# Kernel tuning notes

Measured on AMD Instinct MI355X. Metric: run time of the kernel, lower is better.

Reference implementation:

```python
import jax, jax.numpy as jnp
import numpy as np

N, E, D, V, MAX_EDGES, G, ITERS = 50000, 200000, 128, 2000, 3, 256, 2


def _mlp3(h, W1, b1, W2, b2, W3, b3):
    h = jax.nn.relu(h @ W1 + b1)
    h = jax.nn.relu(h @ W2 + b2)
    return jax.nn.relu(h @ W3 + b3)


def _enc(ids, emb, W1, b1, W2, b2):
    h = emb[ids]
    h = jax.nn.relu(h @ W1 + b1)
    return jax.nn.relu(h @ W2 + b2)


def setup_inputs():
    key = jax.random.key(0)
    ks = iter(jax.random.split(key, 64))

    def p(shape):
        return jax.random.normal(next(ks), shape, jnp.float32) * 0.02

    inp = {
        'x': jax.random.randint(next(ks), (N,), 0, V),
        'edge_index': jax.random.randint(next(ks), (2, E), 0, N),
        'edge_attr': jax.random.randint(next(ks), (E,), 0, MAX_EDGES),
        'batch_vec': jnp.sort(jax.random.randint(next(ks), (N,), 0, G)),
        'emb_node': p((V, 2 * D)), 'Wn1': p((2 * D, D)), 'bn1': jnp.zeros((D,), jnp.float32),
        'Wn2': p((D, D)), 'bn2': jnp.zeros((D,), jnp.float32),
        'emb_edge': p((MAX_EDGES, 2 * D)), 'We1': p((2 * D, D)), 'be1': jnp.zeros((D,), jnp.float32),
        'We2': p((D, D)), 'be2': jnp.zeros((D,), jnp.float32),
    }
    for tag in ('p', 'c', 'f'):  # parent_agg, child_agg, final_agg 3-layer MLPs
        inp['W' + tag + '1'] = p((3 * D, 2 * D)); inp['b' + tag + '1'] = jnp.zeros((2 * D,), jnp.float32)
        inp['W' + tag + '2'] = p((2 * D, D)); inp['b' + tag + '2'] = jnp.zeros((D,), jnp.float32)
        inp['W' + tag + '3'] = p((D, D)); inp['b' + tag + '3'] = jnp.zeros((D,), jnp.float32)
    inp['Wo1'] = p((D, 4 * D)); inp['bo1'] = jnp.zeros((4 * D,), jnp.float32)
    inp['Wo2'] = p((4 * D, 8 * D)); inp['bo2'] = jnp.zeros((8 * D,), jnp.float32)
    return inp


def reference(x, edge_index, edge_attr, batch_vec, emb_node, Wn1, bn1, Wn2, bn2,
              emb_edge, We1, be1, We2, be2,
              Wp1, bp1, Wp2, bp2, Wp3, bp3,
              Wc1, bc1, Wc2, bc2, Wc3, bc3,
              Wf1, bf1, Wf2, bf2, Wf3, bf3,
              Wo1, bo1, Wo2, bo2):
    nodes = _enc(x, emb_node, Wn1, bn1, Wn2, bn2)       # [N, D]
    ea = _enc(edge_attr, emb_edge, We1, be1, We2, be2)  # [E, D]
    src, dst = edge_index[0], edge_index[1]
    # both aggregations normalize by degree of edge_index[0] (as in the source)
    deg = jax.ops.segment_sum(jnp.ones((E,), nodes.dtype), src, num_segments=N)
    deg_inv = jnp.where(deg > 0, 1.0 / deg, 0.0)[:, None]  # [N, 1]
    for _ in range(ITERS):
        # parent agg: flow source_to_target -> x_i = nodes[dst], x_j = nodes[src], sum at dst
        mp = _mlp3(jnp.concatenate([nodes[dst], nodes[src], ea], axis=1), Wp1, bp1, Wp2, bp2, Wp3, bp3)
        fi = deg_inv * jax.ops.segment_sum(mp, dst, num_segments=N)
        # child agg: flow target_to_source -> x_i = nodes[src], x_j = nodes[dst], sum at src
        mc = _mlp3(jnp.concatenate([nodes[src], nodes[dst], ea], axis=1), Wc1, bc1, Wc2, bc2, Wc3, bc3)
        fo = deg_inv * jax.ops.segment_sum(mc, src, num_segments=N)
        upd = _mlp3(jnp.concatenate([nodes, fi, fo], axis=1), Wf1, bf1, Wf2, bf2, Wf3, bf3)
        nodes = nodes + upd
    h = jax.nn.relu(nodes @ Wo1 + bo1)
    h = jax.nn.relu(h @ Wo2 + bo2)                      # [N, 8D]
    return jax.ops.segment_max(h, batch_vec, num_segments=G)  # global max pool [G, 8D]
```

## Files before the change

### kernel.cpp

```cpp
#include <hip/hip_runtime.h>

#define NN 50000
#define NE 200000
#define DD 128
#define GG 256
#define NITERS 2
#define NBINS 50176
#define NPART 196

typedef unsigned short u16;
typedef unsigned int u32;
typedef __bf16 bf16x8 __attribute__((ext_vector_type(8)));
typedef float f32x4 __attribute__((ext_vector_type(4)));

union U16x8 { uint4 u; bf16x8 v; u16 s[8]; };

__device__ __forceinline__ u16 f2b(float f) {
    u32 u = __float_as_uint(f);
    return (u16)((u + 0x7FFFu + ((u >> 16) & 1u)) >> 16);
}
__device__ __forceinline__ float b2f(u16 s) { return __uint_as_float(((u32)s) << 16); }

__device__ __forceinline__ uint2 pack4(const float* v) {
    uint2 r;
    r.x = (u32)f2b(v[0]) | ((u32)f2b(v[1]) << 16);
    r.y = (u32)f2b(v[2]) | ((u32)f2b(v[3]) << 16);
    return r;
}

__device__ __forceinline__ void gload_lds16(const void* g, void* lds) {
    __builtin_amdgcn_global_load_lds((const __attribute__((address_space(1))) void*)g,
                                     (__attribute__((address_space(3))) void*)lds, 16, 0, 0);
}

__device__ __forceinline__ int xcd_swz(int orig, int nwg) {
    int q = nwg >> 3, r = nwg & 7;
    int x = orig & 7, loc = orig >> 3;
    return (x < r ? x * (q + 1) : r * (q + 1) + (x - r) * q) + loc;
}

template<int K, int NL, int EPI, bool RELU, int LDN>
__global__ __launch_bounds__(256) void expand_k(
    const u16* __restrict__ A, const uint4* __restrict__ wfrag,
    const float* __restrict__ bias, float* __restrict__ of, u16* __restrict__ ob,
    float* __restrict__ zf, int M)
{
    constexpr int KS = K / 32;
    __shared__ uint4 smem[K * 16];
    const int t = threadIdx.x, l = t & 63, wv = t >> 6;
    const int mh = wv >> 1, nh = wv & 1;
    const int mblk = blockIdx.x;
    const int c = blockIdx.y;

    #pragma unroll
    for (int i = 0; i < K / 16; ++i) {
        int s = t + 256 * i;
        int ln = s & 63, mt = (s >> 6) & 7, ksl = s >> 9;
        int row = mblk * 128 + mt * 16 + (ln & 15);
        if (row >= M) row = M - 1;
        int kk = ksl * 32 + (ln >> 4) * 8;
        gload_lds16(A + (size_t)row * K + kk, &smem[s - ln]);
    }
    if (zf) {
        #pragma unroll
        for (int i = 0; i < 4; ++i) {
            int f = t + 256 * i;
            int row = f >> 3, c4 = f & 7;
            int grow = mblk * 128 + row;
            if (grow < M) {
                float4 z; z.x = 0.f; z.y = 0.f; z.z = 0.f; z.w = 0.f;
                *(float4*)(zf + (size_t)grow * 128 + c * 32 + c4 * 4) = z;
            }
        }
    }
    __syncthreads();

    f32x4 acc[4][4] = {};
    #pragma unroll
    for (int ksl = 0; ksl < KS; ++ksl) {
        uint4 wa[4];
        #pragma unroll
        for (int mi = 0; mi < 4; ++mi)
            wa[mi] = wfrag[(size_t)((c * KS + ksl) * 8 + mh * 4 + mi) * 64 + l];
        bf16x8 bn[4];
        #pragma unroll
        for (int ni = 0; ni < 4; ++ni) { U16x8 u; u.u = smem[(ksl * 8 + nh * 4 + ni) * 64 + l]; bn[ni] = u.v; }
        #pragma unroll
        for (int mi = 0; mi < 4; ++mi) {
            U16x8 u; u.u = wa[mi];
            #pragma unroll
            for (int ni = 0; ni < 4; ++ni)
                acc[mi][ni] = __builtin_amdgcn_mfma_f32_16x16x32_bf16(u.v, bn[ni], acc[mi][ni], 0, 0, 0);
        }
    }
    float4 bb[4];
    #pragma unroll
    for (int mi = 0; mi < 4; ++mi) {
        if (bias) bb[mi] = *(const float4*)(bias + c * 128 + mh * 64 + mi * 16 + 4 * (l >> 4));
        else { bb[mi].x = 0.f; bb[mi].y = 0.f; bb[mi].z = 0.f; bb[mi].w = 0.f; }
    }
    #pragma unroll
    for (int ni = 0; ni < 4; ++ni) {
        int node = mblk * 128 + nh * 64 + ni * 16 + (l & 15);
        if (node >= M) continue;
        #pragma unroll
        for (int mi = 0; mi < 4; ++mi) {
            int col = c * 128 + mh * 64 + mi * 16 + 4 * (l >> 4);
            float v[4];
            const float* bf = &bb[mi].x;
            #pragma unroll
            for (int r = 0; r < 4; ++r) {
                v[r] = acc[mi][ni][r] + bf[r];
                if (RELU) v[r] = fmaxf(v[r], 0.f);
            }
            if (EPI == 0) {
                *(uint2*)(ob + (size_t)node * LDN + col) = pack4(v);
            } else {
                size_t a = (size_t)node * 128 + col;
                if (EPI == 2) {
                    float4 old = *(const float4*)(of + a);
                    v[0] += old.x; v[1] += old.y; v[2] += old.z; v[3] += old.w;
                }
                float4 s4; s4.x = v[0]; s4.y = v[1]; s4.z = v[2]; s4.w = v[3];
                *(float4*)(of + a) = s4;
                *(uint2*)(ob + a) = pack4(v);
            }
        }
    }
}

struct SrcBf16 {
    static constexpr bool DIRECT = true;
    const u16* A; int K;
    __device__ const void* gaddr(int row, int kk) const { return A + (size_t)row * K + kk; }
    __device__ bf16x8 operator()(int row, int kk) const {
        U16x8 u; u.u = *(const uint4*)(A + (size_t)row * K + kk); return u.v;
    }
};
struct SrcEnc {
    static constexpr bool DIRECT = false;
    const float* emb; const int* xids;
    __device__ const void* gaddr(int, int) const { return nullptr; }
    __device__ bf16x8 operator()(int row, int kk) const {
        int n = xids[row];
        const float* p = emb + (size_t)n * 256 + kk;
        float4 f0 = *(const float4*)p, f1 = *(const float4*)(p + 4);
        U16x8 r;
        r.s[0]=f2b(f0.x); r.s[1]=f2b(f0.y); r.s[2]=f2b(f0.z); r.s[3]=f2b(f0.w);
        r.s[4]=f2b(f1.x); r.s[5]=f2b(f1.y); r.s[6]=f2b(f1.z); r.s[7]=f2b(f1.w);
        return r.v;
    }
};
struct SrcUpd {
    static constexpr bool DIRECT = false;
    const float* nodes; const float* fi; const float* fo; const int* deg;
    __device__ const void* gaddr(int, int) const { return nullptr; }
    __device__ bf16x8 operator()(int row, int kk) const {
        const float* s; float sc = 1.f;
        if (kk < 128) s = nodes + (size_t)row * 128 + kk;
        else {
            int d = deg[row];
            sc = d > 0 ? 1.f / (float)d : 0.f;
            s = (kk < 256) ? fi + (size_t)row * 128 + (kk - 128)
                           : fo + (size_t)row * 128 + (kk - 256);
        }
        float4 f0 = *(const float4*)s, f1 = *(const float4*)(s + 4);
        U16x8 r;
        r.s[0]=f2b(f0.x*sc); r.s[1]=f2b(f0.y*sc); r.s[2]=f2b(f0.z*sc); r.s[3]=f2b(f0.w*sc);
        r.s[4]=f2b(f1.x*sc); r.s[5]=f2b(f1.y*sc); r.s[6]=f2b(f1.z*sc); r.s[7]=f2b(f1.w*sc);
        return r.v;
    }
};

struct EpiArgs { float* of; u16* ob; const int* idx; int ldN; };

template<int KDIM, int NBLK, int EPI, bool RELU, class SRC>
__global__ __launch_bounds__(256) void gemm_k(SRC src, const uint4* __restrict__ wfrag,
                                              const float* __restrict__ bias,
                                              EpiArgs ea, int M)
{
    constexpr int KS = KDIM / 32;
    constexpr int NPANEL = KDIM / 64;
    __shared__ uint4 smem[2048];
    const int t = threadIdx.x;
    const int l = t & 63;
    const int wv = t >> 6;
    const int mh = wv >> 1, nh = wv & 1;
    const int ell = xcd_swz(blockIdx.x, gridDim.x);
    const int mblk = ell / NBLK, nblk = ell % NBLK;

    f32x4 acc[4][4] = {};

    for (int p = 0; p < NPANEL; ++p) {
        __syncthreads();
        if constexpr (SRC::DIRECT) {
            #pragma unroll
            for (int i = 0; i < 4; ++i) {
                int s = t + 256 * i;
                int ln = s & 63, mt = (s >> 6) & 7, ksl = s >> 9;
                int row = mblk * 128 + mt * 16 + (ln & 15);
                if (row >= M) row = M - 1;
                int kk = p * 64 + ksl * 32 + (ln >> 4) * 8;
                gload_lds16(src.gaddr(row, kk), &smem[s - ln]);
            }
        } else {
            #pragma unroll
            for (int i = 0; i < 4; ++i) {
                int s = t + 256 * i;
                int ln = s & 63, mt = (s >> 6) & 7, ksl = s >> 9;
                int row = mblk * 128 + mt * 16 + (ln & 15);
                if (row >= M) row = M - 1;
                int kk = p * 64 + ksl * 32 + (ln >> 4) * 8;
                U16x8 u; u.v = src(row, kk);
                smem[s] = u.u;
            }
        }
        {
            const uint4* wp = wfrag + (size_t)(nblk * KS + 2 * p) * 512;
            #pragma unroll
            for (int i = 0; i < 4; ++i) {
                int s = t + 256 * i;
                gload_lds16(wp + s, &smem[1024 + (s - (s & 63))]);
            }
        }
        __syncthreads();
        #pragma unroll
        for (int ksl = 0; ksl < 2; ++ksl) {
            bf16x8 a[4], b[4];
            #pragma unroll
            for (int mi = 0; mi < 4; ++mi) { U16x8 u; u.u = smem[(ksl*8 + mh*4 + mi)*64 + l]; a[mi] = u.v; }
            #pragma unroll
            for (int ni = 0; ni < 4; ++ni) { U16x8 u; u.u = smem[1024 + (ksl*8 + nh*4 + ni)*64 + l]; b[ni] = u.v; }
            #pragma unroll
            for (int mi = 0; mi < 4; ++mi)
                #pragma unroll
                for (int ni = 0; ni < 4; ++ni)
                    acc[mi][ni] = __builtin_amdgcn_mfma_f32_16x16x32_bf16(a[mi], b[ni], acc[mi][ni], 0, 0, 0);
        }
    }

    float bcol[4];
    #pragma unroll
    for (int ni = 0; ni < 4; ++ni)
        bcol[ni] = bias ? bias[nblk * 128 + nh * 64 + ni * 16 + (l & 15)] : 0.f;

    if constexpr (EPI == 0) {
        __syncthreads();
        u16* bn = (u16*)smem;
        #pragma unroll
        for (int mi = 0; mi < 4; ++mi)
            #pragma unroll
            for (int ni = 0; ni < 4; ++ni)
                #pragma unroll
                for (int r = 0; r < 4; ++r) {
                    int rl = mh * 64 + mi * 16 + (l >> 4) * 4 + r;
                    int cl = nh * 64 + ni * 16 + (l & 15);
                    float v = acc[mi][ni][r] + bcol[ni];
                    if (RELU) v = fmaxf(v, 0.f);
                    int sx = (rl >> 2) & 7;
                    bn[rl * 128 + ((((cl >> 3) ^ sx)) << 3) + (cl & 7)] = f2b(v);
                }
        __syncthreads();
        int row = t >> 1, half = t & 1;
        int grow = mblk * 128 + row;
        if (grow < M) {
            int sx = (row >> 2) & 7;
            uint4* dst = (uint4*)(ea.ob + (size_t)grow * ea.ldN + nblk * 128 + half * 64);
            const uint4* sp = ((const uint4*)bn) + row * 16;
            #pragma unroll
            for (int i = 0; i < 8; ++i) dst[i] = sp[(half * 8 + i) ^ sx];
        }
    } else if constexpr (EPI == 3) {
        int g16[4][4];
        #pragma unroll
        for (int mi = 0; mi < 4; ++mi) {
            int rb = mblk * 128 + mh * 64 + mi * 16 + (l >> 4) * 4;
            #pragma unroll
            for (int r = 0; r < 4; ++r)
                g16[mi][r] = (rb + r < M) ? ea.idx[rb + r] : -1;
        }
        #pragma unroll
        for (int ni = 0; ni < 4; ++ni) {
            int colg = nblk * 128 + nh * 64 + ni * 16 + (l & 15);
            float mv = 0.f; int cg = -1;
            #pragma unroll
            for (int mi = 0; mi < 4; ++mi)
                #pragma unroll
                for (int r = 0; r < 4; ++r) {
                    float v = acc[mi][ni][r] + bcol[ni];
                    if (RELU) v = fmaxf(v, 0.f);
                    int g = g16[mi][r];
                    if (g != cg) {
                        if (cg >= 0) atomicMax((u32*)(ea.of + (size_t)cg * 1024 + colg), __float_as_uint(mv));
                        cg = g; mv = v;
                    } else mv = fmaxf(mv, v);
                }
            if (cg >= 0) atomicMax((u32*)(ea.of + (size_t)cg * 1024 + colg), __float_as_uint(mv));
        }
    }
}

__global__ __launch_bounds__(256) void edge_fused(
    const u16* __restrict__ P, const float* __restrict__ T,
    const uint4* __restrict__ W2f, const float* __restrict__ b2,
    const uint4* __restrict__ W3f, const float* __restrict__ b3,
    const int* __restrict__ idxA, const int* __restrict__ idxB,
    const int* __restrict__ eattr, float* __restrict__ agg)
{
    __shared__ uint4 smA[2048];
    __shared__ int   sidx[3][128];
    __shared__ float sT[768];
    const int t = threadIdx.x;
    const int l = t & 63;
    const int wv = t >> 6;
    const int mh = wv >> 1, nh = wv & 1;
    const int base = xcd_swz(blockIdx.x, gridDim.x) * 128;

    if (t < 128) {
        int e = (base + t < NE) ? base + t : NE - 1;
        sidx[0][t] = idxA[e];
        sidx[1][t] = idxB[e];
        sidx[2][t] = eattr[e];
    }
    for (int i = t; i < 768; i += 256) sT[i] = T[i];
    __syncthreads();

    const int rt0 = wv * 16 + (l & 15);
    const int rt1 = (wv + 4) * 16 + (l & 15);
    const int klo = (l >> 4) * 8;
    const u16* pA[2] = { P + (size_t)sidx[0][rt0] * 512, P + (size_t)sidx[0][rt1] * 512 };
    const u16* pB[2] = { P + (size_t)sidx[1][rt0] * 512 + 256, P + (size_t)sidx[1][rt1] * 512 + 256 };
    const float* pT[2] = { sT + sidx[2][rt0] * 256, sT + sidx[2][rt1] * 256 };

    uint4 ra[4], rb[4];
    #pragma unroll
    for (int i = 0; i < 4; ++i) {
        int kk = (i >> 1) * 32 + klo;
        ra[i] = *(const uint4*)(pA[i & 1] + kk);
        rb[i] = *(const uint4*)(pB[i & 1] + kk);
    }

    f32x4 acc[4][4] = {};
    #pragma unroll
    for (int p = 0; p < 4; ++p) {
        #pragma unroll
        for (int i = 0; i < 4; ++i) {
            int kk = (i >> 1) * 32 + klo;
            U16x8 ua, ub, r;
            ua.u = ra[i]; ub.u = rb[i];
            const float* tb = pT[i & 1] + p * 64 + kk;
            #pragma unroll
            for (int j = 0; j < 8; ++j) {
                float v = b2f(ua.s[j]) + b2f(ub.s[j]) + tb[j];
                r.s[j] = f2b(fmaxf(v, 0.f));
            }
            smA[(p & 1) * 1024 + t + 256 * i] = r.u;
            if (p < 3) {
                int kn = (p + 1) * 64 + kk;
                ra[i] = *(const uint4*)(pA[i & 1] + kn);
                rb[i] = *(const uint4*)(pB[i & 1] + kn);
            }
        }
        asm volatile("s_waitcnt lgkmcnt(0)" ::: "memory");
        __builtin_amdgcn_s_barrier();
        uint4 bw[2][4];
        #pragma unroll
        for (int ksl = 0; ksl < 2; ++ksl)
            #pragma unroll
            for (int ni = 0; ni < 4; ++ni)
                bw[ksl][ni] = W2f[(size_t)((p * 2 + ksl) * 8 + nh * 4 + ni) * 64 + l];
        #pragma unroll
        for (int ksl = 0; ksl < 2; ++ksl) {
            bf16x8 a[4];
            #pragma unroll
            for (int mi = 0; mi < 4; ++mi) { U16x8 u; u.u = smA[(p & 1) * 1024 + (ksl*8 + mh*4 + mi)*64 + l]; a[mi] = u.v; }
            #pragma unroll
            for (int mi = 0; mi < 4; ++mi)
                #pragma unroll
                for (int ni = 0; ni < 4; ++ni) {
                    U16x8 u; u.u = bw[ksl][ni];
                    acc[mi][ni] = __builtin_amdgcn_mfma_f32_16x16x32_bf16(a[mi], u.v, acc[mi][ni], 0, 0, 0);
                }
        }
    }

    float bc2[4];
    #pragma unroll
    for (int ni = 0; ni < 4; ++ni) bc2[ni] = b2[nh * 64 + ni * 16 + (l & 15)];
    __builtin_amdgcn_s_barrier();
    u16* bn = (u16*)smA;
    #pragma unroll
    for (int mi = 0; mi < 4; ++mi)
        #pragma unroll
        for (int ni = 0; ni < 4; ++ni)
            #pragma unroll
            for (int r = 0; r < 4; ++r) {
                int rl = mh * 64 + mi * 16 + (l >> 4) * 4 + r;
                int cl = nh * 64 + ni * 16 + (l & 15);
                float v = fmaxf(acc[mi][ni][r] + bc2[ni], 0.f);
                int sx = (rl >> 2) & 7;
                bn[rl * 128 + (((cl >> 3) ^ sx) << 3) + (cl & 7)] = f2b(v);
            }
    asm volatile("s_waitcnt lgkmcnt(0)" ::: "memory");
    __builtin_amdgcn_s_barrier();

    f32x4 acc2[4][4] = {};
    #pragma unroll
    for (int ks = 0; ks < 4; ++ks) {
        uint4 bw[4];
        #pragma unroll
        for (int ni = 0; ni < 4; ++ni)
            bw[ni] = W3f[(size_t)(ks * 8 + nh * 4 + ni) * 64 + l];
        bf16x8 a[4];
        #pragma unroll
        for (int mi = 0; mi < 4; ++mi) {
            int rl = (mh * 4 + mi) * 16 + (l & 15);
            int c0 = ks * 32 + (l >> 4) * 8;
            int sx = (rl >> 2) & 7;
            U16x8 u; u.u = *(const uint4*)&bn[rl * 128 + (((c0 >> 3) ^ sx) << 3)];
            a[mi] = u.v;
        }
        #pragma unroll
        for (int mi = 0; mi < 4; ++mi)
            #pragma unroll
            for (int ni = 0; ni < 4; ++ni) {
                U16x8 u; u.u = bw[ni];
                acc2[mi][ni] = __builtin_amdgcn_mfma_f32_16x16x32_bf16(a[mi], u.v, acc2[mi][ni], 0, 0, 0);
            }
    }

    float bc3[4];
    #pragma unroll
    for (int ni = 0; ni < 4; ++ni) bc3[ni] = b3[nh * 64 + ni * 16 + (l & 15)];
    #pragma unroll
    for (int mi = 0; mi < 4; ++mi) {
        int rt4 = mh * 64 + mi * 16 + (l >> 4) * 4;
        int nd[4];
        #pragma unroll
        for (int r = 0; r < 4; ++r)
            nd[r] = (base + rt4 + r < NE) ? sidx[0][rt4 + r] : -1;
        #pragma unroll
        for (int ni = 0; ni < 4; ++ni) {
            int col = nh * 64 + ni * 16 + (l & 15);
            float mv = 0.f; int cg = -1;
            #pragma unroll
            for (int r = 0; r < 4; ++r) {
                float v = fmaxf(acc2[mi][ni][r] + bc3[ni], 0.f);
                if (nd[r] != cg) {
                    if (cg >= 0) atomicAdd(agg + (size_t)cg * 128 + col, mv);
                    cg = nd[r]; mv = v;
                } else mv += v;
            }
            if (cg >= 0) atomicAdd(agg + (size_t)cg * 128 + col, mv);
        }
    }
}

__global__ void hist2_kernel(const int* __restrict__ dstI, const int* __restrict__ srcI,
                             int* __restrict__ hist)
{
    int i = blockIdx.x * 256 + threadIdx.x;
    if (i < NE) atomicAdd(&hist[dstI[i]], 1);
    else if (i < 2 * NE) atomicAdd(&hist[NBINS + srcI[i - NE]], 1);
}
__global__ void chunk_sum(const int* __restrict__ h, int* __restrict__ part)
{
    __shared__ int sh[256];
    int t = threadIdx.x, b = blockIdx.x;
    sh[t] = h[b * 256 + t];
    __syncthreads();
    for (int o = 128; o > 0; o >>= 1) { if (t < o) sh[t] += sh[t + o]; __syncthreads(); }
    if (t == 0) part[b] = sh[0];
}
__global__ void scan_part2(int* part)
{
    __shared__ int sh[256];
    int t = threadIdx.x, b = blockIdx.x;
    int* p = part + b * NPART;
    sh[t] = (t < NPART) ? p[t] : 0;
    __syncthreads();
    for (int o = 1; o < 256; o <<= 1) {
        int x = (t >= o) ? sh[t - o] : 0;
        __syncthreads(); sh[t] += x; __syncthreads();
    }
    if (t < NPART) p[t] = (t ? sh[t - 1] : 0) + b * NE;
}
__global__ void mk_cursor(const int* __restrict__ h, const int* __restrict__ part,
                          int* __restrict__ cur)
{
    __shared__ int sh[256];
    int t = threadIdx.x, b = blockIdx.x;
    int v = h[b * 256 + t];
    sh[t] = v;
    __syncthreads();
    for (int o = 1; o < 256; o <<= 1) {
        int x = (t >= o) ? sh[t - o] : 0;
        __syncthreads(); sh[t] += x; __syncthreads();
    }
    cur[b * 256 + t] = part[b] + sh[t] - v;
}
__global__ void sort_scatter2(const int* __restrict__ dstI, const int* __restrict__ srcI,
                              const int* __restrict__ at, int* __restrict__ cur,
                              int* __restrict__ oA, int* __restrict__ oB, int* __restrict__ oC)
{
    int i = blockIdx.x * 256 + threadIdx.x;
    if (i < NE) {
        int k = dstI[i];
        int p = atomicAdd(&cur[k], 1);
        oA[p] = k; oB[p] = srcI[i]; oC[p] = at[i];
    } else if (i < 2 * NE) {
        int e = i - NE;
        int k = srcI[e];
        int p = atomicAdd(&cur[NBINS + k], 1);
        oA[p] = k; oB[p] = dstI[e]; oC[p] = at[e];
    }
}

struct PackPtrs { const float* p[13]; };

__global__ void pack_all(PackPtrs pp, uint4* __restrict__ frag)
{
    int tid = blockIdx.x * 256 + threadIdx.x;
    if (tid >= 126976) return;
    constexpr int NJ = 15;
    const int   start[NJ] = {0,4096,6144,10240,14336,18432,22528,26624,28672,32768,34816,47104,51200,53248,61440};
    const int   fbase[NJ] = {0,4096,6144,6144,14336,14336,22528,26624,28672,32768,34816,47104,51200,53248,61440};
    const short wsel [NJ] = {0,1,2,2,3,3,4,5,6,7,8,9,10,11,12};
    const short ldt  [NJ] = {128,128,256,256,256,256,128,128,128,128,256,128,128,512,1024};
    const short rot  [NJ] = {0,0,0,128,0,128,0,0,0,0,0,0,0,0,0};
    const short cot  [NJ] = {0,0,0,-256,0,-256,0,0,0,0,0,0,0,0,0};
    const short nbst [NJ] = {0,0,0,2,0,2,0,0,0,0,0,0,0,0,0};
    const short kst  [NJ] = {8,4,4,4,4,4,8,4,8,4,12,8,4,4,16};
    int j = 0;
    for (int i = NJ - 1; i >= 1; --i) if (tid >= start[i]) { j = i; break; }
    int rem = tid - start[j];
    int KS = kst[j];
    int nbrel = rem / (KS * 512);
    int r1 = rem % (KS * 512);
    int ks = r1 >> 9;
    int r2 = r1 & 511;
    int nt = r2 >> 6, l = r2 & 63;
    int nb = nbst[j] + nbrel;
    int k  = ks * 32 + (l >> 4) * 8;
    int ld = ldt[j];
    int col = nb * 128 + nt * 16 + (l & 15) + cot[j];
    const float* W = pp.p[wsel[j]];
    U16x8 u;
    #pragma unroll
    for (int jj = 0; jj < 8; ++jj) u.s[jj] = f2b(W[(size_t)(rot[j] + k + jj) * ld + col]);
    frag[fbase[j] + ((size_t)(nb * KS + ks) * 8 + nt) * 64 + l] = u.u;
}

__global__ void enc_tab_kernel(const float* __restrict__ emb_edge,
                               const float* __restrict__ We1, const float* __restrict__ be1,
                               const float* __restrict__ We2, const float* __restrict__ be2,
                               const float* __restrict__ Wp1, const float* __restrict__ bp1,
                               const float* __restrict__ Wc1, const float* __restrict__ bc1,
                               float* __restrict__ Tp, float* __restrict__ Tc)
{
    __shared__ float h1[3][128];
    __shared__ float ea[3][128];
    const int t = threadIdx.x;
    if (t < 128) {
        for (int a = 0; a < 3; ++a) {
            float s = be1[t];
            for (int k = 0; k < 256; ++k) s = fmaf(emb_edge[a * 256 + k], We1[k * 128 + t], s);
            h1[a][t] = fmaxf(s, 0.f);
        }
    }
    __syncthreads();
    if (t < 128) {
        for (int a = 0; a < 3; ++a) {
            float s = be2[t];
            for (int k = 0; k < 128; ++k) s = fmaf(h1[a][k], We2[k * 128 + t], s);
            ea[a][t] = fmaxf(s, 0.f);
        }
    }
    __syncthreads();
    for (int a = 0; a < 3; ++a) {
        float sp = bp1[t], sc = bc1[t];
        for (int k = 0; k < 128; ++k) {
            float e = ea[a][k];
            sp = fmaf(e, Wp1[(size_t)(256 + k) * 256 + t], sp);
            sc = fmaf(e, Wc1[(size_t)(256 + k) * 256 + t], sc);
        }
        Tp[a * 256 + t] = sp;
        Tc[a * 256 + t] = sc;
    }
}

extern "C" void kernel_launch(void* const* d_in, const int* in_sizes, int n_in,
                              void* d_out, int out_size, void* d_ws, size_t ws_size,
                              hipStream_t stream)
{
    const int*   x          = (const int*)d_in[0];
    const int*   edge_index = (const int*)d_in[1];
    const int*   edge_attr  = (const int*)d_in[2];
    const int*   batch_vec  = (const int*)d_in[3];
    const float* emb_node   = (const float*)d_in[4];
    const float* Wn1 = (const float*)d_in[5];  const float* bn1 = (const float*)d_in[6];
    const float* Wn2 = (const float*)d_in[7];  const float* bn2 = (const float*)d_in[8];
    const float* emb_edge = (const float*)d_in[9];
    const float* We1 = (const float*)d_in[10]; const float* be1 = (const float*)d_in[11];
    const float* We2 = (const float*)d_in[12]; const float* be2 = (const float*)d_in[13];
    const float* Wp1 = (const float*)d_in[14]; const float* bp1 = (const float*)d_in[15];
    const float* Wp2 = (const float*)d_in[16]; const float* bp2 = (const float*)d_in[17];
    const float* Wp3 = (const float*)d_in[18]; const float* bp3 = (const float*)d_in[19];
    const float* Wc1 = (const float*)d_in[20]; const float* bc1 = (const float*)d_in[21];
    const float* Wc2 = (const float*)d_in[22]; const float* bc2 = (const float*)d_in[23];
    const float* Wc3 = (const float*)d_in[24]; const float* bc3 = (const float*)d_in[25];
    const float* Wf1 = (const float*)d_in[26]; const float* bf1 = (const float*)d_in[27];
    const float* Wf2 = (const float*)d_in[28]; const float* bf2 = (const float*)d_in[29];
    const float* Wf3 = (const float*)d_in[30]; const float* bf3 = (const float*)d_in[31];
    const float* Wo1 = (const float*)d_in[32]; const float* bo1 = (const float*)d_in[33];
    const float* Wo2 = (const float*)d_in[34]; const float* bo2 = (const float*)d_in[35];

    float* out = (float*)d_out;

    char* w = (char*)d_ws;
    auto alloc = [&](size_t bytes) { char* p = w; w += (bytes + 255) & ~(size_t)255; return p; };
    float* nodes   = (float*)alloc((size_t)NN * DD * 4);
    u16*   nodesbf = (u16*)  alloc((size_t)NN * DD * 2);
    float* fi      = (float*)alloc((size_t)NN * DD * 4);
    float* fo      = (float*)alloc((size_t)NN * DD * 4);
    u16*   P       = (u16*)  alloc((size_t)NN * 512 * 2);
    u16*   h2      = (u16*)  alloc((size_t)NN * 384 * 2);
    float* Tp      = (float*)alloc(3 * 256 * 4);
    float* Tc      = (float*)alloc(3 * 256 * 4);
    uint4* frag    = (uint4*)alloc((size_t)126976 * 16);
    int* hist = (int*)alloc((size_t)2 * NBINS * 4);
    int* part = (int*)alloc((size_t)2 * NPART * 4);
    int* cur  = (int*)alloc((size_t)2 * NBINS * 4);
    int* sA   = (int*)alloc((size_t)2 * NE * 4);
    int* sB   = (int*)alloc((size_t)2 * NE * 4);
    int* sC   = (int*)alloc((size_t)2 * NE * 4);

    u16* He = h2;
    u16* U1 = h2;
    u16* U2 = h2 + (size_t)NN * 256;
    u16* Hout1 = P;
    const int* degS = hist + NBINS;

    uint4* Wn1f = frag;
    uint4* Wn2f = Wn1f + 4096;
    uint4* PWp  = Wn2f + 2048;
    uint4* PWc  = PWp  + 8192;
    uint4* W2p  = PWc  + 8192;
    uint4* W3p  = W2p  + 4096;
    uint4* W2c  = W3p  + 2048;
    uint4* W3c  = W2c  + 4096;
    uint4* Wf1f = W3c  + 2048;
    uint4* Wf2f = Wf1f + 12288;
    uint4* Wf3f = Wf2f + 4096;
    uint4* Wo1f = Wf3f + 2048;
    uint4* Wo2f = Wo1f + 8192;

    const int* srcI = edge_index;
    const int* dstI = edge_index + NE;

    const int MB50 = (NN + 127) / 128;
    const int MBE  = (NE + 127) / 128;

    (void)hipMemsetAsync(d_out, 0, (size_t)out_size * 4, stream);
    (void)hipMemsetAsync(hist, 0, (size_t)2 * NBINS * 4, stream);

    PackPtrs pp;
    pp.p[0]=Wn1; pp.p[1]=Wn2; pp.p[2]=Wp1; pp.p[3]=Wc1; pp.p[4]=Wp2; pp.p[5]=Wp3;
    pp.p[6]=Wc2; pp.p[7]=Wc3; pp.p[8]=Wf1; pp.p[9]=Wf2; pp.p[10]=Wf3; pp.p[11]=Wo1; pp.p[12]=Wo2;
    pack_all<<<(126976 + 255) / 256, 256, 0, stream>>>(pp, frag);

    enc_tab_kernel<<<1, 256, 0, stream>>>(emb_edge, We1, be1, We2, be2,
                                          Wp1, bp1, Wc1, bc1, Tp, Tc);

    hist2_kernel<<<(2 * NE + 255) / 256, 256, 0, stream>>>(dstI, srcI, hist);
    chunk_sum<<<2 * NPART, 256, 0, stream>>>(hist, part);
    scan_part2<<<2, 256, 0, stream>>>(part);
    mk_cursor<<<2 * NPART, 256, 0, stream>>>(hist, part, cur);
    sort_scatter2<<<(2 * NE + 255) / 256, 256, 0, stream>>>(dstI, srcI, edge_attr, cur, sA, sB, sC);

    gemm_k<256, 1, 0, true, SrcEnc><<<MB50, 256, 0, stream>>>(
        SrcEnc{emb_node, x}, Wn1f, bn1, EpiArgs{nullptr, He, nullptr, 128}, NN);
    expand_k<128, 1, 1, true, 128><<<dim3(MB50, 1), 256, 0, stream>>>(
        He, Wn2f, bn2, nodes, nodesbf, nullptr, NN);

    for (int it = 0; it < NITERS; ++it) {
        expand_k<128, 4, 0, false, 512><<<dim3(MB50, 4), 256, 0, stream>>>(
            nodesbf, PWp, nullptr, nullptr, P, fi, NN);
        edge_fused<<<MBE, 256, 0, stream>>>(P, Tp, W2p, bp2, W3p, bp3,
                                            sA, sB, sC, fi);

        expand_k<128, 4, 0, false, 512><<<dim3(MB50, 4), 256, 0, stream>>>(
            nodesbf, PWc, nullptr, nullptr, P, fo, NN);
        edge_fused<<<MBE, 256, 0, stream>>>(P, Tc, W2c, bc2, W3c, bc3,
                                            sA + NE, sB + NE, sC + NE, fo);

        gemm_k<384, 2, 0, true, SrcUpd><<<MB50 * 2, 256, 0, stream>>>(
            SrcUpd{nodes, fi, fo, degS}, Wf1f, bf1, EpiArgs{nullptr, U1, nullptr, 256}, NN);
        gemm_k<256, 1, 0, true, SrcBf16><<<MB50, 256, 0, stream>>>(
            SrcBf16{U1, 256}, Wf2f, bf2, EpiArgs{nullptr, U2, nullptr, 128}, NN);
        expand_k<128, 1, 2, true, 128><<<dim3(MB50, 1), 256, 0, stream>>>(
            U2, Wf3f, bf3, nodes, nodesbf, nullptr, NN);
    }

    expand_k<128, 4, 0, true, 512><<<dim3(MB50, 4), 256, 0, stream>>>(
        nodesbf, Wo1f, bo1, nullptr, Hout1, nullptr, NN);
    gemm_k<512, 8, 3, true, SrcBf16><<<MB50 * 8, 256, 0, stream>>>(
        SrcBf16{Hout1, 512}, Wo2f, bo2, EpiArgs{out, nullptr, batch_vec, 1024}, NN);
}
```

Measured before the change: 903.9 us.

## Batch parent/child edge passes into one launch and fuse update MLP layers

When the workspace is large enough, the parent and child projection GEMMs run as one wide 1024-column expand_k. The two edge_fused passes then run as a single launch with gridDim.y=2, using per-pass parameter structs. Separately, update-MLP layers 2 and 3 are fused into a new upd23 kernel that keeps the intermediate in LDS and does the residual update, removing a launch and the U2 round trip through global memory. This trades twice the P buffer size for fewer launches and more concurrent work, and relies on PWp/PWc and fi/fo being laid out contiguously.

```diff
diff --git a/kernel.cpp b/kernel.cpp
--- a/kernel.cpp
+++ b/kernel.cpp
@@ -62,6 +62,9 @@
         gload_lds16(A + (size_t)row * K + kk, &smem[s - ln]);
     }
     if (zf) {
+        float* zb = zf;
+        int cz = c;
+        if (cz >= 4) { zb += (size_t)NN * 128; cz -= 4; }
         #pragma unroll
         for (int i = 0; i < 4; ++i) {
             int f = t + 256 * i;
@@ -69,7 +72,7 @@
             int grow = mblk * 128 + row;
             if (grow < M) {
                 float4 z; z.x = 0.f; z.y = 0.f; z.z = 0.f; z.w = 0.f;
-                *(float4*)(zf + (size_t)grow * 128 + c * 32 + c4 * 4) = z;
+                *(float4*)(zb + (size_t)grow * 128 + cz * 32 + c4 * 4) = z;
             }
         }
     }
@@ -300,12 +303,126 @@
     }
 }
 
+__global__ __launch_bounds__(256) void upd23(
+    const u16* __restrict__ U1, const uint4* __restrict__ W2f,
+    const float* __restrict__ b2, const uint4* __restrict__ W3f,
+    const float* __restrict__ b3, float* __restrict__ nodes,
+    u16* __restrict__ nodesbf, int M)
+{
+    __shared__ uint4 smem[2048];
+    const int t = threadIdx.x, l = t & 63, wv = t >> 6;
+    const int mh = wv >> 1, nh = wv & 1;
+    const int mblk = xcd_swz(blockIdx.x, gridDim.x);
+
+    f32x4 acc[4][4] = {};
+    for (int p = 0; p < 4; ++p) {
+        __syncthreads();
+        #pragma unroll
+        for (int i = 0; i < 4; ++i) {
+            int s = t + 256 * i;
+            int ln = s & 63, mt = (s >> 6) & 7, ksl = s >> 9;
+            int row = mblk * 128 + mt * 16 + (ln & 15);
+            if (row >= M) row = M - 1;
+            int kk = p * 64 + ksl * 32 + (ln >> 4) * 8;
+            gload_lds16(U1 + (size_t)row * 256 + kk, &smem[s - ln]);
+        }
+        {
+            const uint4* wp = W2f + (size_t)(2 * p) * 512;
+            #pragma unroll
+            for (int i = 0; i < 4; ++i) {
+                int s = t + 256 * i;
+                gload_lds16(wp + s, &smem[1024 + (s - (s & 63))]);
+            }
+        }
+        __syncthreads();
+        #pragma unroll
+        for (int ksl = 0; ksl < 2; ++ksl) {
+            bf16x8 a[4], b[4];
+            #pragma unroll
+            for (int mi = 0; mi < 4; ++mi) { U16x8 u; u.u = smem[(ksl*8 + mh*4 + mi)*64 + l]; a[mi] = u.v; }
+            #pragma unroll
+            for (int ni = 0; ni < 4; ++ni) { U16x8 u; u.u = smem[1024 + (ksl*8 + nh*4 + ni)*64 + l]; b[ni] = u.v; }
+            #pragma unroll
+            for (int mi = 0; mi < 4; ++mi)
+                #pragma unroll
+                for (int ni = 0; ni < 4; ++ni)
+                    acc[mi][ni] = __builtin_amdgcn_mfma_f32_16x16x32_bf16(a[mi], b[ni], acc[mi][ni], 0, 0, 0);
+        }
+    }
+
+    float bc2[4];
+    #pragma unroll
+    for (int ni = 0; ni < 4; ++ni) bc2[ni] = b2[nh * 64 + ni * 16 + (l & 15)];
+    __syncthreads();
+    u16* bn = (u16*)smem;
+    #pragma unroll
+    for (int mi = 0; mi < 4; ++mi)
+        #pragma unroll
+        for (int ni = 0; ni < 4; ++ni)
+            #pragma unroll
+            for (int r = 0; r < 4; ++r) {
+                int rl = mh * 64 + mi * 16 + (l >> 4) * 4 + r;
+                int cl = nh * 64 + ni * 16 + (l & 15);
+                float v = fmaxf(acc[mi][ni][r] + bc2[ni], 0.f);
+                int sx = (rl >> 2) & 7;
+                bn[rl * 128 + (((cl >> 3) ^ sx) << 3) + (cl & 7)] = f2b(v);
+            }
+    __syncthreads();
+
+    f32x4 acc2[4][4] = {};
+    #pragma unroll
+    for (int ks = 0; ks < 4; ++ks) {
+        uint4 bw[4];
+        #pragma unroll
+        for (int ni = 0; ni < 4; ++ni)
+            bw[ni] = W3f[(size_t)(ks * 8 + nh * 4 + ni) * 64 + l];
+        bf16x8 a[4];
+        #pragma unroll
+        for (int mi = 0; mi < 4; ++mi) {
+            int rl = (mh * 4 + mi) * 16 + (l & 15);
+            int c0 = ks * 32 + (l >> 4) * 8;
+            int sx = (rl >> 2) & 7;
+            U16x8 u; u.u = *(const uint4*)&bn[rl * 128 + (((c0 >> 3) ^ sx) << 3)];
+            a[mi] = u.v;
+        }
+        #pragma unroll
+        for (int mi = 0; mi < 4; ++mi)
+            #pragma unroll
+            for (int ni = 0; ni < 4; ++ni) {
+                U16x8 u; u.u = bw[ni];
+                acc2[mi][ni] = __builtin_amdgcn_mfma_f32_16x16x32_bf16(a[mi], u.v, acc2[mi][ni], 0, 0, 0);
+            }
+    }
+
+    float bc3[4];
+    #pragma unroll
+    for (int ni = 0; ni < 4; ++ni) bc3[ni] = b3[nh * 64 + ni * 16 + (l & 15)];
+    #pragma unroll
+    for (int mi = 0; mi < 4; ++mi)
+        #pragma unroll
+        for (int r = 0; r < 4; ++r) {
+            int row = mblk * 128 + mh * 64 + mi * 16 + (l >> 4) * 4 + r;
+            if (row >= M) continue;
+            #pragma unroll
+            for (int ni = 0; ni < 4; ++ni) {
+                int col = nh * 64 + ni * 16 + (l & 15);
+                size_t a = (size_t)row * 128 + col;
+                float v = nodes[a] + fmaxf(acc2[mi][ni][r] + bc3[ni], 0.f);
+                nodes[a] = v;
+                nodesbf[a] = f2b(v);
+            }
+        }
+}
+
+struct EdgePar {
+    const float* T; const uint4* W2f; const float* b2;
+    const uint4* W3f; const float* b3;
+    const int* iA; const int* iB; const int* iC;
+    float* agg; int base;
+};
+
 __global__ __launch_bounds__(256) void edge_fused(
-    const u16* __restrict__ P, const float* __restrict__ T,
-    const uint4* __restrict__ W2f, const float* __restrict__ b2,
-    const uint4* __restrict__ W3f, const float* __restrict__ b3,
-    const int* __restrict__ idxA, const int* __restrict__ idxB,
-    const int* __restrict__ eattr, float* __restrict__ agg)
+    const u16* __restrict__ P, int ldP, EdgePar e0, EdgePar e1)
 {
     __shared__ uint4 smA[2048];
     __shared__ int   sidx[3][128];
@@ -315,21 +432,24 @@
     const int wv = t >> 6;
     const int mh = wv >> 1, nh = wv & 1;
     const int base = xcd_swz(blockIdx.x, gridDim.x) * 128;
+    const EdgePar ep = (blockIdx.y == 0) ? e0 : e1;
 
     if (t < 128) {
         int e = (base + t < NE) ? base + t : NE - 1;
-        sidx[0][t] = idxA[e];
-        sidx[1][t] = idxB[e];
-        sidx[2][t] = eattr[e];
-    }
-    for (int i = t; i < 768; i += 256) sT[i] = T[i];
+        sidx[0][t] = ep.iA[e];
+        sidx[1][t] = ep.iB[e];
+        sidx[2][t] = ep.iC[e];
+    }
+    for (int i = t; i < 768; i += 256) sT[i] = ep.T[i];
     __syncthreads();
 
     const int rt0 = wv * 16 + (l & 15);
     const int rt1 = (wv + 4) * 16 + (l & 15);
     const int klo = (l >> 4) * 8;
-    const u16* pA[2] = { P + (size_t)sidx[0][rt0] * 512, P + (size_t)sidx[0][rt1] * 512 };
-    const u16* pB[2] = { P + (size_t)sidx[1][rt0] * 512 + 256, P + (size_t)sidx[1][rt1] * 512 + 256 };
+    const u16* pA[2] = { P + (size_t)sidx[0][rt0] * ldP + ep.base,
+                         P + (size_t)sidx[0][rt1] * ldP + ep.base };
+    const u16* pB[2] = { P + (size_t)sidx[1][rt0] * ldP + ep.base + 256,
+                         P + (size_t)sidx[1][rt1] * ldP + ep.base + 256 };
     const float* pT[2] = { sT + sidx[2][rt0] * 256, sT + sidx[2][rt1] * 256 };
 
     uint4 ra[4], rb[4];
@@ -368,7 +488,7 @@
         for (int ksl = 0; ksl < 2; ++ksl)
             #pragma unroll
             for (int ni = 0; ni < 4; ++ni)
-                bw[ksl][ni] = W2f[(size_t)((p * 2 + ksl) * 8 + nh * 4 + ni) * 64 + l];
+                bw[ksl][ni] = ep.W2f[(size_t)((p * 2 + ksl) * 8 + nh * 4 + ni) * 64 + l];
         #pragma unroll
         for (int ksl = 0; ksl < 2; ++ksl) {
             bf16x8 a[4];
@@ -386,7 +506,7 @@
 
     float bc2[4];
     #pragma unroll
-    for (int ni = 0; ni < 4; ++ni) bc2[ni] = b2[nh * 64 + ni * 16 + (l & 15)];
+    for (int ni = 0; ni < 4; ++ni) bc2[ni] = ep.b2[nh * 64 + ni * 16 + (l & 15)];
     __builtin_amdgcn_s_barrier();
     u16* bn = (u16*)smA;
     #pragma unroll
@@ -410,7 +530,7 @@
         uint4 bw[4];
         #pragma unroll
         for (int ni = 0; ni < 4; ++ni)
-            bw[ni] = W3f[(size_t)(ks * 8 + nh * 4 + ni) * 64 + l];
+            bw[ni] = ep.W3f[(size_t)(ks * 8 + nh * 4 + ni) * 64 + l];
         bf16x8 a[4];
         #pragma unroll
         for (int mi = 0; mi < 4; ++mi) {
@@ -431,7 +551,7 @@
 
     float bc3[4];
     #pragma unroll
-    for (int ni = 0; ni < 4; ++ni) bc3[ni] = b3[nh * 64 + ni * 16 + (l & 15)];
+    for (int ni = 0; ni < 4; ++ni) bc3[ni] = ep.b3[nh * 64 + ni * 16 + (l & 15)];
     #pragma unroll
     for (int mi = 0; mi < 4; ++mi) {
         int rt4 = mh * 64 + mi * 16 + (l >> 4) * 4;
@@ -447,11 +567,11 @@
             for (int r = 0; r < 4; ++r) {
                 float v = fmaxf(acc2[mi][ni][r] + bc3[ni], 0.f);
                 if (nd[r] != cg) {
-                    if (cg >= 0) atomicAdd(agg + (size_t)cg * 128 + col, mv);
+                    if (cg >= 0) atomicAdd(ep.agg + (size_t)cg * 128 + col, mv);
                     cg = nd[r]; mv = v;
                 } else mv += v;
             }
-            if (cg >= 0) atomicAdd(agg + (size_t)cg * 128 + col, mv);
+            if (cg >= 0) atomicAdd(ep.agg + (size_t)cg * 128 + col, mv);
         }
     }
 }
@@ -617,14 +737,21 @@
 
     float* out = (float*)d_out;
 
+    auto al = [](size_t b) { return (b + 255) & ~(size_t)255; };
+    size_t fixed = al((size_t)NN*DD*4) + al((size_t)NN*DD*2) + al((size_t)NN*DD*4)
+                 + al((size_t)NN*DD*4) + al((size_t)NN*256*2) + 2*al(3*256*4)
+                 + al((size_t)126976*16) + 2*al((size_t)2*NBINS*4) + al((size_t)2*NPART*4)
+                 + 3*al((size_t)2*NE*4);
+    const bool wide = ws_size >= fixed + al((size_t)NN * 1024 * 2);
+
     char* w = (char*)d_ws;
     auto alloc = [&](size_t bytes) { char* p = w; w += (bytes + 255) & ~(size_t)255; return p; };
     float* nodes   = (float*)alloc((size_t)NN * DD * 4);
     u16*   nodesbf = (u16*)  alloc((size_t)NN * DD * 2);
     float* fi      = (float*)alloc((size_t)NN * DD * 4);
     float* fo      = (float*)alloc((size_t)NN * DD * 4);
-    u16*   P       = (u16*)  alloc((size_t)NN * 512 * 2);
-    u16*   h2      = (u16*)  alloc((size_t)NN * 384 * 2);
+    u16*   P       = (u16*)  alloc((size_t)NN * (wide ? 1024 : 512) * 2);
+    u16*   h2      = (u16*)  alloc((size_t)NN * 256 * 2);
     float* Tp      = (float*)alloc(3 * 256 * 4);
     float* Tc      = (float*)alloc(3 * 256 * 4);
     uint4* frag    = (uint4*)alloc((size_t)126976 * 16);
@@ -637,7 +764,6 @@
 
     u16* He = h2;
     u16* U1 = h2;
-    u16* U2 = h2 + (size_t)NN * 256;
     u16* Hout1 = P;
     const int* degS = hist + NBINS;
 
@@ -683,23 +809,27 @@
     expand_k<128, 1, 1, true, 128><<<dim3(MB50, 1), 256, 0, stream>>>(
         He, Wn2f, bn2, nodes, nodesbf, nullptr, NN);
 
+    EdgePar epP = { Tp, W2p, bp2, W3p, bp3, sA,      sB,      sC,      fi, 0 };
+    EdgePar epC = { Tc, W2c, bc2, W3c, bc3, sA + NE, sB + NE, sC + NE, fo, wide ? 512 : 0 };
+
     for (int it = 0; it < NITERS; ++it) {
-        expand_k<128, 4, 0, false, 512><<<dim3(MB50, 4), 256, 0, stream>>>(
-            nodesbf, PWp, nullptr, nullptr, P, fi, NN);
-        edge_fused<<<MBE, 256, 0, stream>>>(P, Tp, W2p, bp2, W3p, bp3,
-                                            sA, sB, sC, fi);
-
-        expand_k<128, 4, 0, false, 512><<<dim3(MB50, 4), 256, 0, stream>>>(
-            nodesbf, PWc, nullptr, nullptr, P, fo, NN);
-        edge_fused<<<MBE, 256, 0, stream>>>(P, Tc, W2c, bc2, W3c, bc3,
-                                            sA + NE, sB + NE, sC + NE, fo);
+        if (wide) {
+            expand_k<128, 8, 0, false, 1024><<<dim3(MB50, 8), 256, 0, stream>>>(
+                nodesbf, PWp, nullptr, nullptr, P, fi, NN);
+            edge_fused<<<dim3(MBE, 2), 256, 0, stream>>>(P, 1024, epP, epC);
+        } else {
+            expand_k<128, 4, 0, false, 512><<<dim3(MB50, 4), 256, 0, stream>>>(
+                nodesbf, PWp, nullptr, nullptr, P, fi, NN);
+            edge_fused<<<dim3(MBE, 1), 256, 0, stream>>>(P, 512, epP, epP);
+            expand_k<128, 4, 0, false, 512><<<dim3(MB50, 4), 256, 0, stream>>>(
+                nodesbf, PWc, nullptr, nullptr, P, fo, NN);
+            EdgePar epC2 = epC;
+            edge_fused<<<dim3(MBE, 1), 256, 0, stream>>>(P, 512, epC2, epC2);
+        }
 
         gemm_k<384, 2, 0, true, SrcUpd><<<MB50 * 2, 256, 0, stream>>>(
             SrcUpd{nodes, fi, fo, degS}, Wf1f, bf1, EpiArgs{nullptr, U1, nullptr, 256}, NN);
-        gemm_k<256, 1, 0, true, SrcBf16><<<MB50, 256, 0, stream>>>(
-            SrcBf16{U1, 256}, Wf2f, bf2, EpiArgs{nullptr, U2, nullptr, 128}, NN);
-        expand_k<128, 1, 2, true, 128><<<dim3(MB50, 1), 256, 0, stream>>>(
-            U2, Wf3f, bf3, nodes, nodesbf, nullptr, NN);
+        upd23<<<MB50, 256, 0, stream>>>(U1, Wf2f, bf2, Wf3f, bf3, nodes, nodesbf, NN);
     }
 
     expand_k<128, 4, 0, true, 512><<<dim3(MB50, 4), 256, 0, stream>>>(
```

Result: faster. 807.4 us (-10.7%).
